# Performance work log

Hardware: AMD Instinct MI355X
Metric: run time of the kernel (lower is better)

Reference implementation:

```python
import jax, jax.numpy as jnp
import numpy as np

DIM = 256
DQK = DIM // 8
LN_SHAPE = (256, 4, 32, 32)


def setup_inputs() -> dict:
    key = jax.random.key(0)
    ks = jax.random.split(key, 12)
    B, C, Z, H, W = 4, 256, 4, 32, 32
    s = 0.02
    return {
        "x": jax.random.normal(ks[0], (B, C, Z, H, W), jnp.float32),
        "y": jax.random.normal(ks[1], (B, C, Z, H, W), jnp.float32),
        "Wq": jax.random.normal(ks[2], (DQK, C), jnp.float32) * s,
        "bq": jnp.zeros((DQK,), jnp.float32),
        "Wk": jax.random.normal(ks[3], (DQK, C), jnp.float32) * s,
        "bk": jnp.zeros((DQK,), jnp.float32),
        "Wv": jax.random.normal(ks[4], (C, C), jnp.float32) * s,
        "bv": jnp.zeros((C,), jnp.float32),
        "W1": jax.random.normal(ks[5], (C, C), jnp.float32) * s,
        "b1": jnp.zeros((C,), jnp.float32),
        "W2": jax.random.normal(ks[6], (C, C), jnp.float32) * s,
        "b2": jnp.zeros((C,), jnp.float32),
        "gamma": jnp.ones(LN_SHAPE, jnp.float32),
        "beta": jnp.zeros(LN_SHAPE, jnp.float32),
    }


def reference(x, y, Wq, bq, Wk, bk, Wv, bv, W1, b1, W2, b2, gamma, beta):
    B, C, Z, H, W = x.shape
    N = Z * H * W
    scale = (C // 8) ** (-0.5)

    def proj(t, Wm, bm):  # 1x1x1 conv3d == channel linear: [B,C,N] -> [B,out,N]
        return jnp.einsum('oc,bcn->bon', Wm, t.reshape(B, C, N)) + bm[None, :, None]

    def branch(a, b):
        q = proj(a, Wq, bq).transpose(0, 2, 1) * scale  # [B,N,dqk]
        k = proj(b, Wk, bk)                             # [B,dqk,N]
        v = proj(b, Wv, bv)                             # [B,C,N]
        attn = jax.nn.softmax(jnp.einsum('bnd,bdm->bnm', q, k), axis=-1)  # [B,N,N]
        out = jnp.einsum('bcm,bnm->bcn', v, attn).reshape(B, C, Z, H, W)
        h = out.transpose(0, 2, 3, 4, 1)  # [B,Z,H,W,C]
        h = jnp.maximum(jnp.einsum('bzhwc,oc->bzhwo', h, W1) + b1, 0.0)
        h = jnp.einsum('bzhwc,oc->bzhwo', h, W2) + b2
        h = h.transpose(0, 4, 1, 2, 3)  # [B,C,Z,H,W]
        mu = h.mean(axis=(1, 2, 3, 4), keepdims=True)
        var = h.var(axis=(1, 2, 3, 4), keepdims=True)
        return (h - mu) / jnp.sqrt(var + 1e-5) * gamma + beta

    return branch(x, y), branch(y, x)
```

## Files before the change

kernel.cpp:

```cpp
#include <hip/hip_runtime.h>

#define C_DIM 256
#define N_TOK 4096
#define DQK_  32
#define SCALE_Q 0.17677669529663687f

typedef unsigned short u16;
typedef __attribute__((ext_vector_type(8))) short bf16x8;
typedef __attribute__((ext_vector_type(16))) float f32x16;

__device__ __forceinline__ u16 f2b(float f) {
  unsigned u = __builtin_bit_cast(unsigned, f);
  unsigned r = (u + 0x7fffu + ((u >> 16) & 1u)) >> 16;
  return (u16)r;
}
__device__ __forceinline__ unsigned splitw(float v) {
  unsigned h = f2b(v);
  float hf = __builtin_bit_cast(float, h << 16);
  unsigned l = f2b(v - hf);
  return h | (l << 16);
}
__device__ __forceinline__ unsigned cvtpk(float lo, float hi) {
  unsigned r;
  asm("v_cvt_pk_bf16_f32 %0, %1, %2" : "=v"(r) : "v"(lo), "v"(hi));
// ... 113 lines not shown
      bf16x8 ah1 = *(const bf16x8*)(ldsAh + (lw + 32 + l31)*128 + (ko ^ swz));
      bf16x8 bh0 = *(const bf16x8*)(ldsBh + (sw + l31)*128      + (ko ^ swz));
      bf16x8 bh1 = *(const bf16x8*)(ldsBh + (sw + 32 + l31)*128 + (ko ^ swz));
      bf16x8 bl0 = *(const bf16x8*)(ldsBl + (sw + l31)*128      + (ko ^ swz));
      bf16x8 bl1 = *(const bf16x8*)(ldsBl + (sw + 32 + l31)*128 + (ko ^ swz));
      acc[0][0] = __builtin_amdgcn_mfma_f32_32x32x16_bf16(ah0, bh0, acc[0][0], 0,0,0);
      acc[0][1] = __builtin_amdgcn_mfma_f32_32x32x16_bf16(ah0, bh1, acc[0][1], 0,0,0);
      acc[1][0] = __builtin_amdgcn_mfma_f32_32x32x16_bf16(ah1, bh0, acc[1][0], 0,0,0);
      acc[1][1] = __builtin_amdgcn_mfma_f32_32x32x16_bf16(ah1, bh1, acc[1][1], 0,0,0);
      acc[0][0] = __builtin_amdgcn_mfma_f32_32x32x16_bf16(ah0, bl0, acc[0][0], 0,0,0);
      acc[0][1] = __builtin_amdgcn_mfma_f32_32x32x16_bf16(ah0, bl1, acc[0][1], 0,0,0);
      acc[1][0] = __builtin_amdgcn_mfma_f32_32x32x16_bf16(ah1, bl0, acc[1][0], 0,0,0);
      acc[1][1] = __builtin_amdgcn_mfma_f32_32x32x16_bf16(ah1, bl1, acc[1][1], 0,0,0);
    }
  }

  for (int h = 0; h < 2; ++h) {
    __syncthreads();
    if ((w >> 1) == h) {
      #pragma unroll
      for (int j = 0; j < 2; ++j) {
        int sl = j*32 + l31;
        float bv = bias[s0 + h*64 + sl];
        #pragma unroll
        for (int i = 0; i < 2; ++i)
          #pragma unroll
          for (int q = 0; q < 4; ++q) {
            int lbase = lw + i*32 + 8*q + 4*g;
            unsigned w0 = (unsigned)f2b(acc[i][j][q*4+0] + bv)
                        | ((unsigned)f2b(acc[i][j][q*4+1] + bv) << 16);
            unsigned w1 = (unsigned)f2b(acc[i][j][q*4+2] + bv)
                        | ((unsigned)f2b(acc[i][j][q*4+3] + bv) << 16);
            *(uint2*)(lds + sl*272 + lbase*2) = make_uint2(w0, w1);
          }
      }
    }
    __syncthreads();
    #pragma unroll
    for (int p = 0; p < 4; ++p) {
      int s = p*16 + (t >> 4), col = (t & 15)*8;
      uint4 v = *(const uint4*)(lds + s*272 + col*2);
      *(uint4*)(Ob + (size_t)(s0 + h*64 + s)*(size_t)N_TOK + l0 + col) = v;
    }
  }
}

__device__ __forceinline__ void proj_qk_body(
    char* lds, int bx, int which, int bb,
    const u16* __restrict__ xs_hi, const u16* __restrict__ ys_hi,
    const u16* __restrict__ Wqh, const u16* __restrict__ Wql,
    const u16* __restrict__ Wkh, const u16* __restrict__ Wkl,
    const float* __restrict__ bq, const float* __restrict__ bk,
    u16* __restrict__ Qout, u16* __restrict__ Kout)
{
  int branch = bb >> 2, batch = bb & 3;
  int n0 = bx * 256;
  const u16* Asrc = (which == 0 ? (branch ? ys_hi : xs_hi) : (branch ? xs_hi : ys_hi))
                    + (size_t)batch * N_TOK * C_DIM;
  const u16* Bh = which ? Wkh : Wqh;
  const u16* Bl = which ? Wkl : Wql;
  const float* bias = which ? bk : bq;
  float sc = which ? 1.0f : SCALE_Q;
  u16* out = (which ? Kout : Qout) + (size_t)bb * N_TOK * DQK_;

  char* ldsA  = lds;
  char* ldsBh = lds + 32768;
  char* ldsBl = lds + 40960;

  int t = threadIdx.x, w = t >> 6, lane = t & 63, g = lane >> 5, l31 = lane & 31;
  int swz = (l31 & 7) << 4;

  f32x16 acc[2];
  #pragma unroll
  for (int i = 0; i < 2; ++i)
    #pragma unroll
    for (int r = 0; r < 16; ++r) acc[i][r] = 0.f;

  uint4 rA[8]; uint4 rBh, rBl;
  #pragma unroll
  for (int c = 0; c < 8; ++c) {
    int idx = c*256 + t, row = idx >> 3, slot = idx & 7;
    rA[c] = *(const uint4*)(Asrc + (size_t)(n0 + row)*C_DIM + slot*8);
  }
  { int row = t >> 3, slot = t & 7;
    rBh = *(const uint4*)(Bh + (size_t)row*C_DIM + slot*8);
    rBl = *(const uint4*)(Bl + (size_t)row*C_DIM + slot*8); }

  for (int bk = 0; bk < 4; ++bk) {
    __syncthreads();
    #pragma unroll
    for (int c = 0; c < 8; ++c) {
      int idx = c*256 + t, row = idx >> 3, slot = idx & 7;
      *(uint4*)(ldsA + row*128 + ((slot*16) ^ ((row & 7) << 4))) = rA[c];
    }
    { int row = t >> 3, slot = t & 7;
      int off = row*128 + ((slot*16) ^ ((row & 7) << 4));
      *(uint4*)(ldsBh + off) = rBh;
      *(uint4*)(ldsBl + off) = rBl; }
    __syncthreads();
    if (bk < 3) {
      #pragma unroll
      for (int c = 0; c < 8; ++c) {
        int idx = c*256 + t, row = idx >> 3, slot = idx & 7;
        rA[c] = *(const uint4*)(Asrc + (size_t)(n0 + row)*C_DIM + (bk+1)*64 + slot*8);
      }
      { int row = t >> 3, slot = t & 7;
        rBh = *(const uint4*)(Bh + (size_t)row*C_DIM + (bk+1)*64 + slot*8);
        rBl = *(const uint4*)(Bl + (size_t)row*C_DIM + (bk+1)*64 + slot*8); }
    }
    #pragma unroll
    for (int ks = 0; ks < 4; ++ks) {
      int ko = ks*32 + g*16;
      bf16x8 a0 = *(const bf16x8*)(ldsA + (w*64 + l31)*128      + (ko ^ swz));
      bf16x8 a1 = *(const bf16x8*)(ldsA + (w*64 + 32 + l31)*128 + (ko ^ swz));
      bf16x8 bh = *(const bf16x8*)(ldsBh + l31*128 + (ko ^ swz));
      bf16x8 bl = *(const bf16x8*)(ldsBl + l31*128 + (ko ^ swz));
      acc[0] = __builtin_amdgcn_mfma_f32_32x32x16_bf16(a0, bh, acc[0], 0,0,0);
      acc[1] = __builtin_amdgcn_mfma_f32_32x32x16_bf16(a1, bh, acc[1], 0,0,0);
      acc[0] = __builtin_amdgcn_mfma_f32_32x32x16_bf16(a0, bl, acc[0], 0,0,0);
      acc[1] = __builtin_amdgcn_mfma_f32_32x32x16_bf16(a1, bl, acc[1], 0,0,0);
    }
  }
  float bv = bias[l31];
  #pragma unroll
  for (int sub = 0; sub < 2; ++sub)
    #pragma unroll
    for (int r = 0; r < 16; ++r) {
      int n = w*64 + sub*32 + (r&3) + 8*(r>>2) + 4*g;
      out[(size_t)(n0 + n)*DQK_ + l31] = f2b((acc[sub][r] + bv) * sc);
    }
}

__global__ __launch_bounds__(256) void pv_qk_kernel(
    const u16* __restrict__ xs_hi, const u16* __restrict__ ys_hi,
    const u16* __restrict__ Wvh, const u16* __restrict__ Wvl,
    const u16* __restrict__ Wqh, const u16* __restrict__ Wql,
    const u16* __restrict__ Wkh, const u16* __restrict__ Wkl,
    const float* __restrict__ bv, const float* __restrict__ bq, const float* __restrict__ bk,
    u16* __restrict__ Vt, u16* __restrict__ Qout, u16* __restrict__ Kout)
{
  __shared__ __align__(16) char lds[49152];
  int bid = blockIdx.x;
  const size_t AS = (size_t)N_TOK * C_DIM;
  if (bid < 512) {
    int bx = bid & 31, by = (bid >> 5) & 1, bb = bid >> 6;
    gemm_v_body(lds, bx, by, bb, ys_hi, xs_hi, AS, Wvh, Wvl, bv, Vt, AS);
  } else {
    int pb = bid - 512;
    int bx = pb & 15, which = (pb >> 4) & 1, bb = pb >> 5;
    proj_qk_body(lds, bx, which, bb, xs_hi, ys_hi, Wqh, Wql, Wkh, Wkl, bq, bk, Qout, Kout);
  }
}

__global__ __launch_bounds__(512) void attn_ffn_kernel(
    const u16* __restrict__ Qg, const u16* __restrict__ Kg,
    const u16* __restrict__ Vtg,
    const u16* __restrict__ W1h, const u16* __restrict__ W1l,
    const u16* __restrict__ W2h, const u16* __restrict__ W2l,
    const float* __restrict__ b1, const float* __restrict__ b2,
    float* __restrict__ out, float* __restrict__ part)
{
  __shared__ __align__(16) char lds[147456];
  int id = blockIdx.x;
  int bb = id & 7;
  int n0 = (id >> 3) * 128;
  const u16* Qb = Qg + (size_t)bb * N_TOK * DQK_;
  const u16* Kb = Kg + (size_t)bb * N_TOK * DQK_;
  const u16* Vb = Vtg + (size_t)bb * C_DIM * N_TOK;

  u16* Kl = (u16*)lds;
  u16* Vl = (u16*)(lds + 16384);

  int t = threadIdx.x;
  int w = t >> 6;
  int grp = w >> 2;
  int wg = w & 3;
  int t4 = t & 255;
  int lane = t & 63, g = lane >> 5, l31 = lane & 31;
  int swz = (l31 & 7) << 4;

  bf16x8 qf0 = *(const bf16x8*)(Qb + (size_t)(n0 + wg*32 + l31)*DQK_ + g*8);
  bf16x8 qf1 = *(const bf16x8*)(Qb + (size_t)(n0 + wg*32 + l31)*DQK_ + 16 + g*8);

  f32x16 acc[8];
  #pragma unroll
  for (int ct = 0; ct < 8; ++ct)
    #pragma unroll
    for (int r = 0; r < 16; ++r) acc[ct][r] = 0.f;

  float L = 0.f;

  bf16x8 stK, stV[8];
  const u16* kSrc = Kb + (size_t)(grp*32*64 + (t4>>7)*32 + (t4&31))*DQK_
                       + ((t4>>6)&1)*16 + ((t4>>5)&1)*8;
  const int vCol0 = grp*32*64;
  stK = *(const bf16x8*)(kSrc);
  #pragma unroll
  for (int i = 0; i < 8; ++i) {
    int q = i*256 + t4;
    stV[i] = *(const bf16x8*)(Vb + (size_t)(q >> 3)*N_TOK + vCol0 + (q & 7)*8);
  }

  u16* VlG = Vl + grp*32768;

  *(bf16x8*)(Kl + grp*4096 + t4*8) = stK;
  #pragma unroll
  for (int i = 0; i < 8; ++i) {
    int q = i*256 + t4;
    int c = q >> 3, slot = q & 7;
    *(bf16x8*)((char*)VlG + c*256 + ((slot*16) ^ ((c & 15) << 4))) = stV[i];
  }
  __syncthreads();

  int h = 0;
  for (int mt = 0; mt < 32; ++mt) {
    const u16* KlG = Kl + grp*4096 + h*2048;
    f32x16 z;
    #pragma unroll
    for (int r = 0; r < 16; ++r) z[r] = 0.f;
    bf16x8 ka = *(const bf16x8*)(KlG + (0*64 + lane)*8);
    bf16x8 kb = *(const bf16x8*)(KlG + (1*64 + lane)*8);
    bf16x8 kc = *(const bf16x8*)(KlG + (2*64 + lane)*8);
    bf16x8 kd = *(const bf16x8*)(KlG + (3*64 + lane)*8);
    f32x16 st0 = __builtin_amdgcn_mfma_f32_32x32x16_bf16(ka, qf0, z, 0,0,0);
    st0 = __builtin_amdgcn_mfma_f32_32x32x16_bf16(kb, qf1, st0, 0,0,0);
    f32x16 st1 = __builtin_amdgcn_mfma_f32_32x32x16_bf16(kc, qf0, z, 0,0,0);
    st1 = __builtin_amdgcn_mfma_f32_32x32x16_bf16(kd, qf1, st1, 0,0,0);

    if (mt + 1 < 32) {
      stK = *(const bf16x8*)(kSrc + (size_t)(mt+1)*64*DQK_);
      #pragma unroll
      for (int i = 0; i < 8; ++i) {
        int q = i*256 + t4;
        stV[i] = *(const bf16x8*)(Vb + (size_t)(q >> 3)*N_TOK + vCol0 + (mt+1)*64 + (q & 7)*8);
      }
    }

    float ps = 0.f;
    uint4 pav[4];
    #pragma unroll
    for (int msub = 0; msub < 2; ++msub) {
      f32x16 sv = msub ? st1 : st0;
      float p[16];
      #pragma unroll
      for (int r = 0; r < 16; ++r)
        p[r] = __expf(fminf(sv[r], 30.f));
      float q0 = (p[0]+p[1]) + (p[2]+p[3]);
      float q1 = (p[4]+p[5]) + (p[6]+p[7]);
      float q2 = (p[8]+p[9]) + (p[10]+p[11]);
      float q3 = (p[12]+p[13]) + (p[14]+p[15]);
      ps += (q0+q1) + (q2+q3);
      unsigned k0a = cvtpk(p[0],  p[1]),  k0b = cvtpk(p[2],  p[3]);
      unsigned k1a = cvtpk(p[4],  p[5]),  k1b = cvtpk(p[6],  p[7]);
      unsigned k2a = cvtpk(p[8],  p[9]),  k2b = cvtpk(p[10], p[11]);
      unsigned k3a = cvtpk(p[12], p[13]), k3b = cvtpk(p[14], p[15]);
      unsigned X1a = g ? k0a : k1a, X1b = g ? k0b : k1b;
      unsigned X2a = g ? k2a : k3a, X2b = g ? k2b : k3b;
      X1a = __shfl_xor(X1a, 32); X1b = __shfl_xor(X1b, 32);
      X2a = __shfl_xor(X2a, 32); X2b = __shfl_xor(X2b, 32);
      pav[msub*2]     = g ? make_uint4(X1a, X1b, k1a, k1b)
                          : make_uint4(k0a, k0b, X1a, X1b);
      pav[msub*2 + 1] = g ? make_uint4(X2a, X2b, k3a, k3b)
                          : make_uint4(k2a, k2b, X2a, X2b);
    }
    ps += __shfl_xor(ps, 32);
    L += ps;

    __builtin_amdgcn_s_setprio(1);
    #pragma unroll
    for (int ks = 0; ks < 4; ++ks) {
      bf16x8 pa = __builtin_bit_cast(bf16x8, pav[ks]);
      #pragma unroll
      for (int ct = 0; ct < 8; ++ct) {
        bf16x8 vv = *(const bf16x8*)((char*)VlG + (ct*32 + l31)*256
                     + ((h*128 + ks*32 + g*16) ^ ((l31 & 15) << 4)));
        acc[ct] = __builtin_amdgcn_mfma_f32_32x32x16_bf16(pa, vv, acc[ct], 0,0,0);
      }
    }
    __builtin_amdgcn_s_setprio(0);

    if (mt + 1 < 32) {
      *(bf16x8*)(Kl + grp*4096 + (h^1)*2048 + t4*8) = stK;
      #pragma unroll
      for (int i = 0; i < 8; ++i) {
        int q = i*256 + t4;
        int c = q >> 3, slot = q & 7;
        *(bf16x8*)((char*)VlG + c*256 + (((h ^ 1)*128 + slot*16) ^ ((c & 15) << 4))) = stV[i];
      }
    }
    __syncthreads();
    h ^= 1;
  }

  float* mb = (float*)Kl;
  mb[t] = L;
  __syncthreads();
  float Ln = L + mb[t ^ 256];

  float* vb = (float*)Vl;
  #pragma unroll
  for (int pass = 0; pass < 2; ++pass) {
    __syncthreads();
    if (grp == 1) {
      #pragma unroll
      for (int cc = 0; cc < 4; ++cc) {
        int ct = pass*4 + cc;
        #pragma unroll
        for (int r = 0; r < 16; ++r)
          vb[(cc*256 + t4)*16 + r] = acc[ct][r];
      }
    }
    __syncthreads();
    if (grp == 0) {
      #pragma unroll
      for (int cc = 0; cc < 4; ++cc) {
        int ct = pass*4 + cc;
        #pragma unroll
        for (int r = 0; r < 16; ++r)
          acc[ct][r] += vb[(cc*256 + t4)*16 + r];
      }
    }
  }
  __syncthreads();

  char* ldsO = lds + 16384;
  if (grp == 0) {
    float lr = 1.0f / Ln;
    float lrr[16];
    #pragma unroll
    for (int r = 0; r < 16; ++r)
      lrr[r] = __shfl(lr, (r&3) + 8*(r>>2) + 4*g, 32);
    #pragma unroll
    for (int ct = 0; ct < 8; ++ct) {
      #pragma unroll
      for (int r = 0; r < 16; ++r) {
        int n = wg*32 + (r&3) + 8*(r>>2) + 4*g;
        int c = ct*32 + l31;
        *(u16*)(ldsO + n*512 + ((c*2) ^ ((n & 7) << 4))) = f2b(acc[ct][r] * lrr[r]);
      }
    }
  }
  __syncthreads();

  int lw = (w & 1) * 64, sw = (w >> 1) * 64;
  char* ldsH1  = lds + 81920;
  char* ldsBh1 = lds + 81920;
  char* ldsBl1 = lds + 114688;
  char* ldsBh2 = lds + 16384;
  char* ldsBl2 = lds + 49152;

  f32x16 fa[2][2];
  #pragma unroll
  for (int i = 0; i < 2; ++i)
    #pragma unroll
    for (int j = 0; j < 2; ++j)
      #pragma unroll
      for (int r = 0; r < 16; ++r) fa[i][j][r] = 0.f;

  uint4 rBh[4], rBl[4];
  #pragma unroll
  for (int c = 0; c < 4; ++c) {
    int u = c*512 + t, row = u >> 3, slot = u & 7;
    rBh[c] = *(const uint4*)(W1h + (size_t)row*C_DIM + slot*8);
    rBl[c] = *(const uint4*)(W1l + (size_t)row*C_DIM + slot*8);
  }
  for (int bk = 0; bk < 4; ++bk) {
    __syncthreads();
    #pragma unroll
    for (int c = 0; c < 4; ++c) {
      int u = c*512 + t, row = u >> 3, slot = u & 7;
      int off = row*128 + ((slot*16) ^ ((row & 7) << 4));
      *(uint4*)(ldsBh1 + off) = rBh[c];
      *(uint4*)(ldsBl1 + off) = rBl[c];
    }
    __syncthreads();
    if (bk < 3) {
      #pragma unroll
      for (int c = 0; c < 4; ++c) {
        int u = c*512 + t, row = u >> 3, slot = u & 7;
        rBh[c] = *(const uint4*)(W1h + (size_t)row*C_DIM + (bk+1)*64 + slot*8);
        rBl[c] = *(const uint4*)(W1l + (size_t)row*C_DIM + (bk+1)*64 + slot*8);
      }
    }
    #pragma unroll
    for (int ks = 0; ks < 4; ++ks) {
      int ko = ks*32 + g*16;
      int kb = bk*128 + ko;
      bf16x8 ah0 = *(const bf16x8*)(ldsO + (lw + l31)*512      + (kb ^ swz));
      bf16x8 ah1 = *(const bf16x8*)(ldsO + (lw + 32 + l31)*512 + (kb ^ swz));
      bf16x8 bh0 = *(const bf16x8*)(ldsBh1 + (sw + l31)*128      + (ko ^ swz));
      bf16x8 bh1 = *(const bf16x8*)(ldsBh1 + (sw + 32 + l31)*128 + (ko ^ swz));
      bf16x8 bl0 = *(const bf16x8*)(ldsBl1 + (sw + l31)*128      + (ko ^ swz));
      bf16x8 bl1 = *(const bf16x8*)(ldsBl1 + (sw + 32 + l31)*128 + (ko ^ swz));
      fa[0][0] = __builtin_amdgcn_mfma_f32_32x32x16_bf16(ah0, bh0, fa[0][0], 0,0,0);
      fa[0][1] = __builtin_amdgcn_mfma_f32_32x32x16_bf16(ah0, bh1, fa[0][1], 0,0,0);
      fa[1][0] = __builtin_amdgcn_mfma_f32_32x32x16_bf16(ah1, bh0, fa[1][0], 0,0,0);
      fa[1][1] = __builtin_amdgcn_mfma_f32_32x32x16_bf16(ah1, bh1, fa[1][1], 0,0,0);
      fa[0][0] = __builtin_amdgcn_mfma_f32_32x32x16_bf16(ah0, bl0, fa[0][0], 0,0,0);
      fa[0][1] = __builtin_amdgcn_mfma_f32_32x32x16_bf16(ah0, bl1, fa[0][1], 0,0,0);
      fa[1][0] = __builtin_amdgcn_mfma_f32_32x32x16_bf16(ah1, bl0, fa[1][0], 0,0,0);
      fa[1][1] = __builtin_amdgcn_mfma_f32_32x32x16_bf16(ah1, bl1, fa[1][1], 0,0,0);
    }
  }
  __syncthreads();

  #pragma unroll
  for (int j = 0; j < 2; ++j) {
    int o = sw + j*32 + l31;
    float bvv = b1[o];
    #pragma unroll
    for (int i = 0; i < 2; ++i)
      #pragma unroll
      for (int r = 0; r < 16; ++r) {
        int n = lw + i*32 + (r&3) + 8*(r>>2) + 4*g;
        *(u16*)(ldsH1 + n*512 + ((o*2) ^ ((n & 7) << 4))) = f2b(fmaxf(fa[i][j][r] + bvv, 0.f));
      }
  }

  #pragma unroll
  for (int i = 0; i < 2; ++i)
    #pragma unroll
    for (int j = 0; j < 2; ++j)
      #pragma unroll
      for (int r = 0; r < 16; ++r) fa[i][j][r] = 0.f;

  #pragma unroll
  for (int c = 0; c < 4; ++c) {
    int u = c*512 + t, row = u >> 3, slot = u & 7;
    rBh[c] = *(const uint4*)(W2h + (size_t)row*C_DIM + slot*8);
    rBl[c] = *(const uint4*)(W2l + (size_t)row*C_DIM + slot*8);
  }
  for (int bk = 0; bk < 4; ++bk) {
    __syncthreads();
    #pragma unroll
    for (int c = 0; c < 4; ++c) {
      int u = c*512 + t, row = u >> 3, slot = u & 7;
      int off = row*128 + ((slot*16) ^ ((row & 7) << 4));
      *(uint4*)(ldsBh2 + off) = rBh[c];
      *(uint4*)(ldsBl2 + off) = rBl[c];
    }
    __syncthreads();
    if (bk < 3) {
      #pragma unroll
      for (int c = 0; c < 4; ++c) {
        int u = c*512 + t, row = u >> 3, slot = u & 7;
        rBh[c] = *(const uint4*)(W2h + (size_t)row*C_DIM + (bk+1)*64 + slot*8);
        rBl[c] = *(const uint4*)(W2l + (size_t)row*C_DIM + (bk+1)*64 + slot*8);
      }
    }
    #pragma unroll
    for (int ks = 0; ks < 4; ++ks) {
      int ko = ks*32 + g*16;
      int kb = bk*128 + ko;
      bf16x8 ah0 = *(const bf16x8*)(ldsH1 + (lw + l31)*512      + (kb ^ swz));
      bf16x8 ah1 = *(const bf16x8*)(ldsH1 + (lw + 32 + l31)*512 + (kb ^ swz));
      bf16x8 bh0 = *(const bf16x8*)(ldsBh2 + (sw + l31)*128      + (ko ^ swz));
      bf16x8 bh1 = *(const bf16x8*)(ldsBh2 + (sw + 32 + l31)*128 + (ko ^ swz));
      bf16x8 bl0 = *(const bf16x8*)(ldsBl2 + (sw + l31)*128      + (ko ^ swz));
      bf16x8 bl1 = *(const bf16x8*)(ldsBl2 + (sw + 32 + l31)*128 + (ko ^ swz));
      fa[0][0] = __builtin_amdgcn_mfma_f32_32x32x16_bf16(ah0, bh0, fa[0][0], 0,0,0);
      fa[0][1] = __builtin_amdgcn_mfma_f32_32x32x16_bf16(ah0, bh1, fa[0][1], 0,0,0);
      fa[1][0] = __builtin_amdgcn_mfma_f32_32x32x16_bf16(ah1, bh0, fa[1][0], 0,0,0);
      fa[1][1] = __builtin_amdgcn_mfma_f32_32x32x16_bf16(ah1, bh1, fa[1][1], 0,0,0);
      fa[0][0] = __builtin_amdgcn_mfma_f32_32x32x16_bf16(ah0, bl0, fa[0][0], 0,0,0);
      fa[0][1] = __builtin_amdgcn_mfma_f32_32x32x16_bf16(ah0, bl1, fa[0][1], 0,0,0);
      fa[1][0] = __builtin_amdgcn_mfma_f32_32x32x16_bf16(ah1, bl0, fa[1][0], 0,0,0);
      fa[1][1] = __builtin_amdgcn_mfma_f32_32x32x16_bf16(ah1, bl1, fa[1][1], 0,0,0);
    }
  }

  float s = 0.f, s2 = 0.f;
  #pragma unroll
  for (int j = 0; j < 2; ++j) {
    float bvv = b2[sw + j*32 + l31];
    #pragma unroll
    for (int i = 0; i < 2; ++i)
      #pragma unroll
      for (int r = 0; r < 16; ++r) {
        fa[i][j][r] += bvv;
        s += fa[i][j][r];
        s2 += fa[i][j][r]*fa[i][j][r];
      }
  }
  for (int off = 32; off; off >>= 1) {
    s  += __shfl_down(s, off, 64);
    s2 += __shfl_down(s2, off, 64);
  }
  __syncthreads();
  float* sc = (float*)lds;
  if (lane == 0) { sc[w*2] = s; sc[w*2+1] = s2; }
  __syncthreads();
  if (t == 0) {
    int slot = bb*32 + (id >> 3);
    float S = 0.f, S2 = 0.f;
    #pragma unroll
    for (int q = 0; q < 8; ++q) { S += sc[q*2]; S2 += sc[q*2+1]; }
    part[slot*2]     = S;
    part[slot*2 + 1] = S2;
  }

  float* Ob = out + (size_t)bb * (size_t)N_TOK * C_DIM;
  int l0 = n0;
  for (int qp = 0; qp < 4; ++qp) {
    __syncthreads();
    if ((w >> 1) == qp) {
      #pragma unroll
      for (int j = 0; j < 2; ++j) {
        int sl = j*32 + l31;
        #pragma unroll
        for (int i = 0; i < 2; ++i)
          #pragma unroll
          for (int q = 0; q < 4; ++q) {
            int lbase = lw + i*32 + 8*q + 4*g;
            float4 vv;
            vv.x = fa[i][j][q*4+0];
            vv.y = fa[i][j][q*4+1];
            vv.z = fa[i][j][q*4+2];
            vv.w = fa[i][j][q*4+3];
            *(float4*)(ldsO + sl*528 + lbase*4) = vv;
          }
      }
    }
    __syncthreads();
    #pragma unroll
    for (int p2 = 0; p2 < 4; ++p2) {
      int idx = p2*512 + t;
      int sl = idx >> 5, col = (idx & 31)*4;
      float4 v = *(const float4*)(ldsO + sl*528 + col*4);
      *(float4*)(Ob + (size_t)(qp*64 + sl)*(size_t)N_TOK + l0 + col) = v;
    }
  }
}

__global__ __launch_bounds__(256) void ln_apply_kernel(
    float* __restrict__ H, const float* __restrict__ gamma,
    const float* __restrict__ beta, const float* __restrict__ part)
{
  __shared__ float st[2];
  int base = blockIdx.x * 4096;
  int bb = base >> 20;
  int t = threadIdx.x;
  if (t < 64) {
    float s = 0.f, s2 = 0.f;
    if (t < 32) { s = part[(bb*32 + t)*2]; s2 = part[(bb*32 + t)*2 + 1]; }
    for (int off = 16; off; off >>= 1) {
      s  += __shfl_down(s, off, 64);
      s2 += __shfl_down(s2, off, 64);
    }
    if (t == 0) {
      float mean = s * (1.0f/1048576.0f);
      float var  = s2 * (1.0f/1048576.0f) - mean*mean;
      st[0] = mean;
      st[1] = rsqrtf(var + 1e-5f);
    }
  }
  __syncthreads();
  float mean = st[0], istd = st[1];
  #pragma unroll
  for (int k = 0; k < 4; ++k) {
    int e = base + (k*256 + t)*4;
    int rem = e & ((1 << 20) - 1);
    float4 h = *(float4*)(H + (size_t)e);
    float4 g = *(const float4*)(gamma + rem);
    float4 b = *(const float4*)(beta + rem);
    h.x = (h.x - mean)*istd*g.x + b.x;
    h.y = (h.y - mean)*istd*g.y + b.y;
    h.z = (h.z - mean)*istd*g.z + b.z;
    h.w = (h.w - mean)*istd*g.w + b.w;
    *(float4*)(H + (size_t)e) = h;
  }
}

extern "C" void kernel_launch(void* const* d_in, const int* in_sizes, int n_in,
                              void* d_out, int out_size, void* d_ws, size_t ws_size,
                              hipStream_t stream) {
  (void)in_sizes; (void)n_in; (void)out_size; (void)ws_size;
  const float* x  = (const float*)d_in[0];
  const float* y  = (const float*)d_in[1];
  const float* Wq = (const float*)d_in[2];
  const float* bq = (const float*)d_in[3];
  const float* Wk = (const float*)d_in[4];
  const float* bk = (const float*)d_in[5];
  const float* Wv = (const float*)d_in[6];
  const float* bv = (const float*)d_in[7];
  const float* W1 = (const float*)d_in[8];
  const float* b1 = (const float*)d_in[9];
  const float* W2 = (const float*)d_in[10];
  const float* b2 = (const float*)d_in[11];
  const float* gamma = (const float*)d_in[12];
  const float* beta  = (const float*)d_in[13];
  float* out = (float*)d_out;

  char* ws = (char*)d_ws;
  u16* xs_hi = (u16*)(ws);
  u16* ys_hi = (u16*)(ws + (8ull<<20));
  u16* Q     = (u16*)(ws + (16ull<<20));
  u16* Kp    = (u16*)(ws + (18ull<<20));
  u16* Vt    = (u16*)(ws + (20ull<<20));
  u16* Wvh   = (u16*)(ws + (52ull<<20));
  u16* Wvl   = Wvh + 65536;
  u16* W1h   = Wvh + 2*65536;
  u16* W1l   = Wvh + 3*65536;
  u16* W2h   = Wvh + 4*65536;
  u16* W2l   = Wvh + 5*65536;
  u16* Wqh   = Wvh + 6*65536;
  u16* Wql   = Wqh + 8192;
  u16* Wkh   = Wqh + 2*8192;
  u16* Wkl   = Wqh + 3*8192;
  float* part  = (float*)(ws + (53ull<<20));

  prep_kernel <<<2880, 256, 0, stream>>>(
      x, y, xs_hi, ys_hi, Wv, W1, W2, Wq, Wk,
      Wvh, Wvl, W1h, W1l, W2h, W2l, Wqh, Wql, Wkh, Wkl);
  pv_qk_kernel<<<768, 256, 0, stream>>>(
      xs_hi, ys_hi, Wvh, Wvl, Wqh, Wql, Wkh, Wkl, bv, bq, bk, Vt, Q, Kp);
  attn_ffn_kernel<<<256, 512, 0, stream>>>(
      Q, Kp, Vt, W1h, W1l, W2h, W2l, b1, b2, out, part);
  ln_apply_kernel <<<2048, 256, 0, stream>>>(out, gamma, beta, part);
}
```

Baseline: 218.3 us.

## Halve attention-FFN query tile to 64 tokens and double grid for occupancy

```diff
diff --git a/kernel.cpp b/kernel.cpp
--- a/kernel.cpp
+++ b/kernel.cpp
@@ -289,7 +289,7 @@
   }
 }
 
-__global__ __launch_bounds__(512) void attn_ffn_kernel(
+__global__ __launch_bounds__(512, 4) void attn_ffn_kernel(
     const u16* __restrict__ Qg, const u16* __restrict__ Kg,
     const u16* __restrict__ Vtg,
     const u16* __restrict__ W1h, const u16* __restrict__ W1l,
@@ -297,132 +297,134 @@
     const float* __restrict__ b1, const float* __restrict__ b2,
     float* __restrict__ out, float* __restrict__ part)
 {
-  __shared__ __align__(16) char lds[147456];
+  __shared__ __align__(16) char lds[73728];
   int id = blockIdx.x;
   int bb = id & 7;
-  int n0 = (id >> 3) * 128;
+  int tile = id >> 3;
+  int n0 = tile * 64;
   const u16* Qb = Qg + (size_t)bb * N_TOK * DQK_;
   const u16* Kb = Kg + (size_t)bb * N_TOK * DQK_;
   const u16* Vb = Vtg + (size_t)bb * C_DIM * N_TOK;
 
   u16* Kl = (u16*)lds;
-  u16* Vl = (u16*)(lds + 16384);
+  u16* Vl = (u16*)(lds + 8192);
 
   int t = threadIdx.x;
   int w = t >> 6;
   int grp = w >> 2;
-  int wg = w & 3;
+  int ch  = (w >> 1) & 1;
+  int qs  = w & 1;
   int t4 = t & 255;
   int lane = t & 63, g = lane >> 5, l31 = lane & 31;
-  int swz = (l31 & 7) << 4;
-
-  bf16x8 qf0 = *(const bf16x8*)(Qb + (size_t)(n0 + wg*32 + l31)*DQK_ + g*8);
-  bf16x8 qf1 = *(const bf16x8*)(Qb + (size_t)(n0 + wg*32 + l31)*DQK_ + 16 + g*8);
-
-  f32x16 acc[8];
-  #pragma unroll
-  for (int ct = 0; ct < 8; ++ct)
+
+  bf16x8 qf0 = *(const bf16x8*)(Qb + (size_t)(n0 + qs*32 + l31)*DQK_ + g*8);
+  bf16x8 qf1 = *(const bf16x8*)(Qb + (size_t)(n0 + qs*32 + l31)*DQK_ + 16 + g*8);
+
+  f32x16 acc[4];
+  #pragma unroll
+  for (int ct = 0; ct < 4; ++ct)
     #pragma unroll
     for (int r = 0; r < 16; ++r) acc[ct][r] = 0.f;
 
   float L = 0.f;
 
-  bf16x8 stK, stV[8];
-  const u16* kSrc = Kb + (size_t)(grp*32*64 + (t4>>7)*32 + (t4&31))*DQK_
-                       + ((t4>>6)&1)*16 + ((t4>>5)&1)*8;
-  const int vCol0 = grp*32*64;
-  stK = *(const bf16x8*)(kSrc);
-  #pragma unroll
-  for (int i = 0; i < 8; ++i) {
+  int kchunk = t4 >> 1, khalf = t4 & 1;
+  const u16* kSrc = Kb + (size_t)(grp*2048 + (kchunk & 31))*DQK_
+                      + ((kchunk>>6)&1)*16 + ((kchunk>>5)&1)*8 + khalf*4;
+  const int vCol0 = grp*2048;
+  u16* KlG0 = Kl + grp*2048;
+  u16* VlG  = Vl + grp*16384;
+
+  uint2 stK = *(const uint2*)(kSrc);
+  uint4 stV[4];
+  #pragma unroll
+  for (int i = 0; i < 4; ++i) {
     int q = i*256 + t4;
-    stV[i] = *(const bf16x8*)(Vb + (size_t)(q >> 3)*N_TOK + vCol0 + (q & 7)*8);
-  }
-
-  u16* VlG = Vl + grp*32768;
-
-  *(bf16x8*)(Kl + grp*4096 + t4*8) = stK;
-  #pragma unroll
-  for (int i = 0; i < 8; ++i) {
+    int c = q >> 2, slot = q & 3;
+    stV[i] = *(const uint4*)(Vb + (size_t)c*N_TOK + vCol0 + slot*8);
+  }
+
+  *(uint2*)(KlG0 + kchunk*8 + khalf*4) = stK;
+  #pragma unroll
+  for (int i = 0; i < 4; ++i) {
     int q = i*256 + t4;
-    int c = q >> 3, slot = q & 7;
-    *(bf16x8*)((char*)VlG + c*256 + ((slot*16) ^ ((c & 15) << 4))) = stV[i];
+    int c = q >> 2, slot = q & 3;
+    *(uint4*)((char*)VlG + c*128 + ((slot*16) ^ ((c & 7) << 4))) = stV[i];
   }
   __syncthreads();
 
   int h = 0;
-  for (int mt = 0; mt < 32; ++mt) {
-    const u16* KlG = Kl + grp*4096 + h*2048;
+  for (int mt = 0; mt < 64; ++mt) {
+    const u16* KlG = KlG0 + h*1024;
     f32x16 z;
     #pragma unroll
     for (int r = 0; r < 16; ++r) z[r] = 0.f;
-    bf16x8 ka = *(const bf16x8*)(KlG + (0*64 + lane)*8);
-    bf16x8 kb = *(const bf16x8*)(KlG + (1*64 + lane)*8);
-    bf16x8 kc = *(const bf16x8*)(KlG + (2*64 + lane)*8);
-    bf16x8 kd = *(const bf16x8*)(KlG + (3*64 + lane)*8);
+    bf16x8 ka = *(const bf16x8*)(KlG + lane*8);
+    bf16x8 kb = *(const bf16x8*)(KlG + (64 + lane)*8);
     f32x16 st0 = __builtin_amdgcn_mfma_f32_32x32x16_bf16(ka, qf0, z, 0,0,0);
     st0 = __builtin_amdgcn_mfma_f32_32x32x16_bf16(kb, qf1, st0, 0,0,0);
-    f32x16 st1 = __builtin_amdgcn_mfma_f32_32x32x16_bf16(kc, qf0, z, 0,0,0);
-    st1 = __builtin_amdgcn_mfma_f32_32x32x16_bf16(kd, qf1, st1, 0,0,0);
-
-    if (mt + 1 < 32) {
-      stK = *(const bf16x8*)(kSrc + (size_t)(mt+1)*64*DQK_);
-      #pragma unroll
-      for (int i = 0; i < 8; ++i) {
+
+    if (mt + 1 < 64) {
+      stK = *(const uint2*)(kSrc + (size_t)(mt+1)*32*DQK_);
+      #pragma unroll
+      for (int i = 0; i < 4; ++i) {
         int q = i*256 + t4;
-        stV[i] = *(const bf16x8*)(Vb + (size_t)(q >> 3)*N_TOK + vCol0 + (mt+1)*64 + (q & 7)*8);
-      }
-    }
-
-    float ps = 0.f;
-    uint4 pav[4];
-    #pragma unroll
-    for (int msub = 0; msub < 2; ++msub) {
-      f32x16 sv = msub ? st1 : st0;
-      float p[16];
-      #pragma unroll
-      for (int r = 0; r < 16; ++r)
-        p[r] = __expf(fminf(sv[r], 30.f));
-      float q0 = (p[0]+p[1]) + (p[2]+p[3]);
-      float q1 = (p[4]+p[5]) + (p[6]+p[7]);
-      float q2 = (p[8]+p[9]) + (p[10]+p[11]);
-      float q3 = (p[12]+p[13]) + (p[14]+p[15]);
-      ps += (q0+q1) + (q2+q3);
-      unsigned k0a = cvtpk(p[0],  p[1]),  k0b = cvtpk(p[2],  p[3]);
-      unsigned k1a = cvtpk(p[4],  p[5]),  k1b = cvtpk(p[6],  p[7]);
-      unsigned k2a = cvtpk(p[8],  p[9]),  k2b = cvtpk(p[10], p[11]);
-      unsigned k3a = cvtpk(p[12], p[13]), k3b = cvtpk(p[14], p[15]);
+        int c = q >> 2, slot = q & 3;
+        stV[i] = *(const uint4*)(Vb + (size_t)c*N_TOK + vCol0 + (mt+1)*32 + slot*8);
+      }
+    }
+
+    float ps;
+    uint4 pav[2];
+    {
+      float p0 = __expf(fminf(st0[0], 30.f)),  p1 = __expf(fminf(st0[1], 30.f));
+      float p2 = __expf(fminf(st0[2], 30.f)),  p3 = __expf(fminf(st0[3], 30.f));
+      unsigned k0a = cvtpk(p0, p1), k0b = cvtpk(p2, p3);
+      float s01 = (p0+p1) + (p2+p3);
+      float p4 = __expf(fminf(st0[4], 30.f)),  p5 = __expf(fminf(st0[5], 30.f));
+      float p6 = __expf(fminf(st0[6], 30.f)),  p7 = __expf(fminf(st0[7], 30.f));
+      unsigned k1a = cvtpk(p4, p5), k1b = cvtpk(p6, p7);
+      float s23 = (p4+p5) + (p6+p7);
+      float p8 = __expf(fminf(st0[8], 30.f)),  p9 = __expf(fminf(st0[9], 30.f));
+      float pa2 = __expf(fminf(st0[10], 30.f)), pb2 = __expf(fminf(st0[11], 30.f));
+      unsigned k2a = cvtpk(p8, p9), k2b = cvtpk(pa2, pb2);
+      float s45 = (p8+p9) + (pa2+pb2);
+      float pc2 = __expf(fminf(st0[12], 30.f)), pd2 = __expf(fminf(st0[13], 30.f));
+      float pe2 = __expf(fminf(st0[14], 30.f)), pf2 = __expf(fminf(st0[15], 30.f));
+      unsigned k3a = cvtpk(pc2, pd2), k3b = cvtpk(pe2, pf2);
+      float s67 = (pc2+pd2) + (pe2+pf2);
+      ps = (s01 + s23) + (s45 + s67);
       unsigned X1a = g ? k0a : k1a, X1b = g ? k0b : k1b;
       unsigned X2a = g ? k2a : k3a, X2b = g ? k2b : k3b;
       X1a = __shfl_xor(X1a, 32); X1b = __shfl_xor(X1b, 32);
       X2a = __shfl_xor(X2a, 32); X2b = __shfl_xor(X2b, 32);
-      pav[msub*2]     = g ? make_uint4(X1a, X1b, k1a, k1b)
-                          : make_uint4(k0a, k0b, X1a, X1b);
-      pav[msub*2 + 1] = g ? make_uint4(X2a, X2b, k3a, k3b)
-                          : make_uint4(k2a, k2b, X2a, X2b);
+      pav[0] = g ? make_uint4(X1a, X1b, k1a, k1b) : make_uint4(k0a, k0b, X1a, X1b);
+      pav[1] = g ? make_uint4(X2a, X2b, k3a, k3b) : make_uint4(k2a, k2b, X2a, X2b);
     }
     ps += __shfl_xor(ps, 32);
     L += ps;
 
     __builtin_amdgcn_s_setprio(1);
     #pragma unroll
-    for (int ks = 0; ks < 4; ++ks) {
+    for (int ks = 0; ks < 2; ++ks) {
       bf16x8 pa = __builtin_bit_cast(bf16x8, pav[ks]);
       #pragma unroll
-      for (int ct = 0; ct < 8; ++ct) {
-        bf16x8 vv = *(const bf16x8*)((char*)VlG + (ct*32 + l31)*256
-                     + ((h*128 + ks*32 + g*16) ^ ((l31 & 15) << 4)));
+      for (int ct = 0; ct < 4; ++ct) {
+        int cr = ch*128 + ct*32 + l31;
+        bf16x8 vv = *(const bf16x8*)((char*)VlG + cr*128
+                     + ((h*64 + ks*32 + g*16) ^ ((l31 & 7) << 4)));
         acc[ct] = __builtin_amdgcn_mfma_f32_32x32x16_bf16(pa, vv, acc[ct], 0,0,0);
       }
     }
     __builtin_amdgcn_s_setprio(0);
 
-    if (mt + 1 < 32) {
-      *(bf16x8*)(Kl + grp*4096 + (h^1)*2048 + t4*8) = stK;
-      #pragma unroll
-      for (int i = 0; i < 8; ++i) {
+    if (mt + 1 < 64) {
+      *(uint2*)(KlG0 + (h^1)*1024 + kchunk*8 + khalf*4) = stK;
+      #pragma unroll
+      for (int i = 0; i < 4; ++i) {
         int q = i*256 + t4;
-        int c = q >> 3, slot = q & 7;
-        *(bf16x8*)((char*)VlG + c*256 + (((h ^ 1)*128 + slot*16) ^ ((c & 15) << 4))) = stV[i];
+        int c = q >> 2, slot = q & 3;
+        *(uint4*)((char*)VlG + c*128 + (((h^1)*64 + slot*16) ^ ((c & 7) << 4))) = stV[i];
       }
     }
     __syncthreads();
@@ -430,37 +432,28 @@
   }
 
   float* mb = (float*)Kl;
+  float* vb = (float*)Vl;
   mb[t] = L;
+  if (grp == 1) {
+    #pragma unroll
+    for (int ct = 0; ct < 4; ++ct)
+      #pragma unroll
+      for (int r = 0; r < 16; ++r)
+        vb[(ct*256 + t4)*16 + r] = acc[ct][r];
+  }
   __syncthreads();
-  float Ln = L + mb[t ^ 256];
-
-  float* vb = (float*)Vl;
-  #pragma unroll
-  for (int pass = 0; pass < 2; ++pass) {
-    __syncthreads();
-    if (grp == 1) {
-      #pragma unroll
-      for (int cc = 0; cc < 4; ++cc) {
-        int ct = pass*4 + cc;
-        #pragma unroll
-        for (int r = 0; r < 16; ++r)
-          vb[(cc*256 + t4)*16 + r] = acc[ct][r];
-      }
-    }
-    __syncthreads();
-    if (grp == 0) {
-      #pragma unroll
-      for (int cc = 0; cc < 4; ++cc) {
-        int ct = pass*4 + cc;
-        #pragma unroll
-        for (int r = 0; r < 16; ++r)
-          acc[ct][r] += vb[(cc*256 + t4)*16 + r];
-      }
-    }
+  float Ln = 1.f;
+  if (grp == 0) {
+    Ln = L + mb[t ^ 256];
+    #pragma unroll
+    for (int ct = 0; ct < 4; ++ct)
+      #pragma unroll
+      for (int r = 0; r < 16; ++r)
+        acc[ct][r] += vb[(ct*256 + t4)*16 + r];
   }
   __syncthreads();
 
-  char* ldsO = lds + 16384;
+  char* ldsO = lds + 8192;
   if (grp == 0) {
     float lr = 1.0f / Ln;
     float lrr[16];
@@ -468,156 +461,135 @@
     for (int r = 0; r < 16; ++r)
       lrr[r] = __shfl(lr, (r&3) + 8*(r>>2) + 4*g, 32);
     #pragma unroll
-    for (int ct = 0; ct < 8; ++ct) {
+    for (int ct = 0; ct < 4; ++ct) {
       #pragma unroll
       for (int r = 0; r < 16; ++r) {
-        int n = wg*32 + (r&3) + 8*(r>>2) + 4*g;
-        int c = ct*32 + l31;
+        int n = qs*32 + (r&3) + 8*(r>>2) + 4*g;
+        int c = ch*128 + ct*32 + l31;
         *(u16*)(ldsO + n*512 + ((c*2) ^ ((n & 7) << 4))) = f2b(acc[ct][r] * lrr[r]);
       }
     }
   }
   __syncthreads();
 
-  int lw = (w & 1) * 64, sw = (w >> 1) * 64;
-  char* ldsH1  = lds + 81920;
-  char* ldsBh1 = lds + 81920;
-  char* ldsBl1 = lds + 114688;
-  char* ldsBh2 = lds + 16384;
-  char* ldsBl2 = lds + 49152;
-
-  f32x16 fa[2][2];
-  #pragma unroll
-  for (int i = 0; i < 2; ++i)
-    #pragma unroll
-    for (int j = 0; j < 2; ++j)
-      #pragma unroll
-      for (int r = 0; r < 16; ++r) fa[i][j][r] = 0.f;
-
-  uint4 rBh[4], rBl[4];
-  #pragma unroll
-  for (int c = 0; c < 4; ++c) {
-    int u = c*512 + t, row = u >> 3, slot = u & 7;
-    rBh[c] = *(const uint4*)(W1h + (size_t)row*C_DIM + slot*8);
-    rBl[c] = *(const uint4*)(W1l + (size_t)row*C_DIM + slot*8);
-  }
-  for (int bk = 0; bk < 4; ++bk) {
-    __syncthreads();
-    #pragma unroll
-    for (int c = 0; c < 4; ++c) {
-      int u = c*512 + t, row = u >> 3, slot = u & 7;
-      int off = row*128 + ((slot*16) ^ ((row & 7) << 4));
-      *(uint4*)(ldsBh1 + off) = rBh[c];
-      *(uint4*)(ldsBl1 + off) = rBl[c];
-    }
-    __syncthreads();
-    if (bk < 3) {
-      #pragma unroll
-      for (int c = 0; c < 4; ++c) {
-        int u = c*512 + t, row = u >> 3, slot = u & 7;
-        rBh[c] = *(const uint4*)(W1h + (size_t)row*C_DIM + (bk+1)*64 + slot*8);
-        rBl[c] = *(const uint4*)(W1l + (size_t)row*C_DIM + (bk+1)*64 + slot*8);
-      }
-    }
-    #pragma unroll
-    for (int ks = 0; ks < 4; ++ks) {
+  int lw = w & 1, sq = w >> 1;
+  char* ldsWh = lds + 40960;
+  char* ldsWl = lds + 57344;
+  char* ldsH1 = lds + 8192;
+  int swz3 = (l31 & 3) << 4;
+  int swz7 = (l31 & 7) << 4;
+
+  f32x16 fa[2];
+  #pragma unroll
+  for (int j = 0; j < 2; ++j)
+    #pragma unroll
+    for (int r = 0; r < 16; ++r) fa[j][r] = 0.f;
+
+  uint4 rWh[2], rWl[2];
+  #pragma unroll
+  for (int c2 = 0; c2 < 2; ++c2) {
+    int u = c2*512 + t, s = u >> 2, slot = u & 3;
+    rWh[c2] = *(const uint4*)(W1h + (size_t)s*C_DIM + slot*8);
+    rWl[c2] = *(const uint4*)(W1l + (size_t)s*C_DIM + slot*8);
+  }
+  for (int bk = 0; bk < 8; ++bk) {
+    __syncthreads();
+    #pragma unroll
+    for (int c2 = 0; c2 < 2; ++c2) {
+      int u = c2*512 + t, s = u >> 2, slot = u & 3;
+      int off = s*64 + ((slot*16) ^ ((s & 3) << 4));
+      *(uint4*)(ldsWh + off) = rWh[c2];
+      *(uint4*)(ldsWl + off) = rWl[c2];
+    }
+    __syncthreads();
+    if (bk < 7) {
+      #pragma unroll
+      for (int c2 = 0; c2 < 2; ++c2) {
+        int u = c2*512 + t, s = u >> 2, slot = u & 3;
+        rWh[c2] = *(const uint4*)(W1h + (size_t)s*C_DIM + (bk+1)*32 + slot*8);
+        rWl[c2] = *(const uint4*)(W1l + (size_t)s*C_DIM + (bk+1)*32 + slot*8);
+      }
+    }
+    #pragma unroll
+    for (int ks = 0; ks < 2; ++ks) {
       int ko = ks*32 + g*16;
-      int kb = bk*128 + ko;
-      bf16x8 ah0 = *(const bf16x8*)(ldsO + (lw + l31)*512      + (kb ^ swz));
-      bf16x8 ah1 = *(const bf16x8*)(ldsO + (lw + 32 + l31)*512 + (kb ^ swz));
-      bf16x8 bh0 = *(const bf16x8*)(ldsBh1 + (sw + l31)*128      + (ko ^ swz));
-      bf16x8 bh1 = *(const bf16x8*)(ldsBh1 + (sw + 32 + l31)*128 + (ko ^ swz));
-      bf16x8 bl0 = *(const bf16x8*)(ldsBl1 + (sw + l31)*128      + (ko ^ swz));
-      bf16x8 bl1 = *(const bf16x8*)(ldsBl1 + (sw + 32 + l31)*128 + (ko ^ swz));
-      fa[0][0] = __builtin_amdgcn_mfma_f32_32x32x16_bf16(ah0, bh0, fa[0][0], 0,0,0);
-      fa[0][1] = __builtin_amdgcn_mfma_f32_32x32x16_bf16(ah0, bh1, fa[0][1], 0,0,0);
-      fa[1][0] = __builtin_amdgcn_mfma_f32_32x32x16_bf16(ah1, bh0, fa[1][0], 0,0,0);
-      fa[1][1] = __builtin_amdgcn_mfma_f32_32x32x16_bf16(ah1, bh1, fa[1][1], 0,0,0);
-      fa[0][0] = __builtin_amdgcn_mfma_f32_32x32x16_bf16(ah0, bl0, fa[0][0], 0,0,0);
-      fa[0][1] = __builtin_amdgcn_mfma_f32_32x32x16_bf16(ah0, bl1, fa[0][1], 0,0,0);
-      fa[1][0] = __builtin_amdgcn_mfma_f32_32x32x16_bf16(ah1, bl0, fa[1][0], 0,0,0);
-      fa[1][1] = __builtin_amdgcn_mfma_f32_32x32x16_bf16(ah1, bl1, fa[1][1], 0,0,0);
+      bf16x8 a0  = *(const bf16x8*)(ldsO + (lw*32 + l31)*512 + ((bk*64 + ko) ^ swz7));
+      bf16x8 bh0 = *(const bf16x8*)(ldsWh + (sq*64 + l31)*64      + (ko ^ swz3));
+      bf16x8 bh1 = *(const bf16x8*)(ldsWh + (sq*64 + 32 + l31)*64 + (ko ^ swz3));
+      bf16x8 bl0 = *(const bf16x8*)(ldsWl + (sq*64 + l31)*64      + (ko ^ swz3));
+      bf16x8 bl1 = *(const bf16x8*)(ldsWl + (sq*64 + 32 + l31)*64 + (ko ^ swz3));
+      fa[0] = __builtin_amdgcn_mfma_f32_32x32x16_bf16(a0, bh0, fa[0], 0,0,0);
+      fa[1] = __builtin_amdgcn_mfma_f32_32x32x16_bf16(a0, bh1, fa[1], 0,0,0);
+      fa[0] = __builtin_amdgcn_mfma_f32_32x32x16_bf16(a0, bl0, fa[0], 0,0,0);
+      fa[1] = __builtin_amdgcn_mfma_f32_32x32x16_bf16(a0, bl1, fa[1], 0,0,0);
     }
   }
   __syncthreads();
 
   #pragma unroll
-  for (int j = 0; j < 2; ++j) {
-    int o = sw + j*32 + l31;
-    float bvv = b1[o];
-    #pragma unroll
-    for (int i = 0; i < 2; ++i)
-      #pragma unroll
-      for (int r = 0; r < 16; ++r) {
-        int n = lw + i*32 + (r&3) + 8*(r>>2) + 4*g;
-        *(u16*)(ldsH1 + n*512 + ((o*2) ^ ((n & 7) << 4))) = f2b(fmaxf(fa[i][j][r] + bvv, 0.f));
-      }
-  }
-
-  #pragma unroll
-  for (int i = 0; i < 2; ++i)
-    #pragma unroll
-    for (int j = 0; j < 2; ++j)
-      #pragma unroll
-      for (int r = 0; r < 16; ++r) fa[i][j][r] = 0.f;
-
-  #pragma unroll
-  for (int c = 0; c < 4; ++c) {
-    int u = c*512 + t, row = u >> 3, slot = u & 7;
-    rBh[c] = *(const uint4*)(W2h + (size_t)row*C_DIM + slot*8);
-    rBl[c] = *(const uint4*)(W2l + (size_t)row*C_DIM + slot*8);
-  }
-  for (int bk = 0; bk < 4; ++bk) {
-    __syncthreads();
-    #pragma unroll
-    for (int c = 0; c < 4; ++c) {
-      int u = c*512 + t, row = u >> 3, slot = u & 7;
-      int off = row*128 + ((slot*16) ^ ((row & 7) << 4));
-      *(uint4*)(ldsBh2 + off) = rBh[c];
-      *(uint4*)(ldsBl2 + off) = rBl[c];
-    }
-    __syncthreads();
-    if (bk < 3) {
-      #pragma unroll
-      for (int c = 0; c < 4; ++c) {
-        int u = c*512 + t, row = u >> 3, slot = u & 7;
-        rBh[c] = *(const uint4*)(W2h + (size_t)row*C_DIM + (bk+1)*64 + slot*8);
-        rBl[c] = *(const uint4*)(W2l + (size_t)row*C_DIM + (bk+1)*64 + slot*8);
-      }
-    }
-    #pragma unroll
-    for (int ks = 0; ks < 4; ++ks) {
+  for (int jb = 0; jb < 2; ++jb) {
+    int s = sq*64 + jb*32 + l31;
+    float bvv = b1[s];
+    #pragma unroll
+    for (int r = 0; r < 16; ++r) {
+      int n = lw*32 + (r&3) + 8*(r>>2) + 4*g;
+      *(u16*)(ldsH1 + n*512 + ((s*2) ^ ((n & 7) << 4))) = f2b(fmaxf(fa[jb][r] + bvv, 0.f));
+    }
+  }
+  #pragma unroll
+  for (int j = 0; j < 2; ++j)
+    #pragma unroll
+    for (int r = 0; r < 16; ++r) fa[j][r] = 0.f;
+
+  #pragma unroll
+  for (int c2 = 0; c2 < 2; ++c2) {
+    int u = c2*512 + t, s = u >> 2, slot = u & 3;
+    rWh[c2] = *(const uint4*)(W2h + (size_t)s*C_DIM + slot*8);
+    rWl[c2] = *(const uint4*)(W2l + (size_t)s*C_DIM + slot*8);
+  }
+  for (int bk = 0; bk < 8; ++bk) {
+    __syncthreads();
+    #pragma unroll
+    for (int c2 = 0; c2 < 2; ++c2) {
+      int u = c2*512 + t, s = u >> 2, slot = u & 3;
+      int off = s*64 + ((slot*16) ^ ((s & 3) << 4));
+      *(uint4*)(ldsWh + off) = rWh[c2];
+      *(uint4*)(ldsWl + off) = rWl[c2];
+    }
+    __syncthreads();
+    if (bk < 7) {
+      #pragma unroll
+      for (int c2 = 0; c2 < 2; ++c2) {
+        int u = c2*512 + t, s = u >> 2, slot = u & 3;
+        rWh[c2] = *(const uint4*)(W2h + (size_t)s*C_DIM + (bk+1)*32 + slot*8);
+        rWl[c2] = *(const uint4*)(W2l + (size_t)s*C_DIM + (bk+1)*32 + slot*8);
+      }
+    }
+    #pragma unroll
+    for (int ks = 0; ks < 2; ++ks) {
       int ko = ks*32 + g*16;
-      int kb = bk*128 + ko;
-      bf16x8 ah0 = *(const bf16x8*)(ldsH1 + (lw + l31)*512      + (kb ^ swz));
-      bf16x8 ah1 = *(const bf16x8*)(ldsH1 + (lw + 32 + l31)*512 + (kb ^ swz));
-      bf16x8 bh0 = *(const bf16x8*)(ldsBh2 + (sw + l31)*128      + (ko ^ swz));
-      bf16x8 bh1 = *(const bf16x8*)(ldsBh2 + (sw + 32 + l31)*128 + (ko ^ swz));
-      bf16x8 bl0 = *(const bf16x8*)(ldsBl2 + (sw + l31)*128      + (ko ^ swz));
-      bf16x8 bl1 = *(const bf16x8*)(ldsBl2 + (sw + 32 + l31)*128 + (ko ^ swz));
-      fa[0][0] = __builtin_amdgcn_mfma_f32_32x32x16_bf16(ah0, bh0, fa[0][0], 0,0,0);
-      fa[0][1] = __builtin_amdgcn_mfma_f32_32x32x16_bf16(ah0, bh1, fa[0][1], 0,0,0);
-      fa[1][0] = __builtin_amdgcn_mfma_f32_32x32x16_bf16(ah1, bh0, fa[1][0], 0,0,0);
-      fa[1][1] = __builtin_amdgcn_mfma_f32_32x32x16_bf16(ah1, bh1, fa[1][1], 0,0,0);
-      fa[0][0] = __builtin_amdgcn_mfma_f32_32x32x16_bf16(ah0, bl0, fa[0][0], 0,0,0);
-      fa[0][1] = __builtin_amdgcn_mfma_f32_32x32x16_bf16(ah0, bl1, fa[0][1], 0,0,0);
-      fa[1][0] = __builtin_amdgcn_mfma_f32_32x32x16_bf16(ah1, bl0, fa[1][0], 0,0,0);
-      fa[1][1] = __builtin_amdgcn_mfma_f32_32x32x16_bf16(ah1, bl1, fa[1][1], 0,0,0);
+      bf16x8 a0  = *(const bf16x8*)(ldsH1 + (lw*32 + l31)*512 + ((bk*64 + ko) ^ swz7));
+      bf16x8 bh0 = *(const bf16x8*)(ldsWh + (sq*64 + l31)*64      + (ko ^ swz3));
+      bf16x8 bh1 = *(const bf16x8*)(ldsWh + (sq*64 + 32 + l31)*64 + (ko ^ swz3));
+      bf16x8 bl0 = *(const bf16x8*)(ldsWl + (sq*64 + l31)*64      + (ko ^ swz3));
+      bf16x8 bl1 = *(const bf16x8*)(ldsWl + (sq*64 + 32 + l31)*64 + (ko ^ swz3));
+      fa[0] = __builtin_amdgcn_mfma_f32_32x32x16_bf16(a0, bh0, fa[0], 0,0,0);
+      fa[1] = __builtin_amdgcn_mfma_f32_32x32x16_bf16(a0, bh1, fa[1], 0,0,0);
+      fa[0] = __builtin_amdgcn_mfma_f32_32x32x16_bf16(a0, bl0, fa[0], 0,0,0);
+      fa[1] = __builtin_amdgcn_mfma_f32_32x32x16_bf16(a0, bl1, fa[1], 0,0,0);
     }
   }
 
   float s = 0.f, s2 = 0.f;
   #pragma unroll
-  for (int j = 0; j < 2; ++j) {
-    float bvv = b2[sw + j*32 + l31];
-    #pragma unroll
-    for (int i = 0; i < 2; ++i)
-      #pragma unroll
-      for (int r = 0; r < 16; ++r) {
-        fa[i][j][r] += bvv;
-        s += fa[i][j][r];
-        s2 += fa[i][j][r]*fa[i][j][r];
-      }
+  for (int jb = 0; jb < 2; ++jb) {
+    float bvv = b2[sq*64 + jb*32 + l31];
+    #pragma unroll
+    for (int r = 0; r < 16; ++r) {
+      fa[jb][r] += bvv;
+      s += fa[jb][r];
+      s2 += fa[jb][r]*fa[jb][r];
+    }
   }
   for (int off = 32; off; off >>= 1) {
     s  += __shfl_down(s, off, 64);
@@ -628,7 +600,7 @@
   if (lane == 0) { sc[w*2] = s; sc[w*2+1] = s2; }
   __syncthreads();
   if (t == 0) {
-    int slot = bb*32 + (id >> 3);
+    int slot = bb*64 + tile;
     float S = 0.f, S2 = 0.f;
     #pragma unroll
     for (int q = 0; q < 8; ++q) { S += sc[q*2]; S2 += sc[q*2+1]; }
@@ -637,34 +609,32 @@
   }
 
   float* Ob = out + (size_t)bb * (size_t)N_TOK * C_DIM;
-  int l0 = n0;
+  char* ts = lds + 40960;
   for (int qp = 0; qp < 4; ++qp) {
     __syncthreads();
-    if ((w >> 1) == qp) {
-      #pragma unroll
-      for (int j = 0; j < 2; ++j) {
-        int sl = j*32 + l31;
+    if (sq == qp) {
+      #pragma unroll
+      for (int jb = 0; jb < 2; ++jb) {
+        int sl = jb*32 + l31;
         #pragma unroll
-        for (int i = 0; i < 2; ++i)
-          #pragma unroll
-          for (int q = 0; q < 4; ++q) {
-            int lbase = lw + i*32 + 8*q + 4*g;
-            float4 vv;
-            vv.x = fa[i][j][q*4+0];
-            vv.y = fa[i][j][q*4+1];
-            vv.z = fa[i][j][q*4+2];
-            vv.w = fa[i][j][q*4+3];
-            *(float4*)(ldsO + sl*528 + lbase*4) = vv;
-          }
-      }
-    }
-    __syncthreads();
-    #pragma unroll
-    for (int p2 = 0; p2 < 4; ++p2) {
+        for (int q2 = 0; q2 < 4; ++q2) {
+          int nbase = lw*32 + 8*q2 + 4*g;
+          float4 vv;
+          vv.x = fa[jb][q2*4+0];
+          vv.y = fa[jb][q2*4+1];
+          vv.z = fa[jb][q2*4+2];
+          vv.w = fa[jb][q2*4+3];
+          *(float4*)(ts + sl*272 + nbase*4) = vv;
+        }
+      }
+    }
+    __syncthreads();
+    #pragma unroll
+    for (int p2 = 0; p2 < 2; ++p2) {
       int idx = p2*512 + t;
-      int sl = idx >> 5, col = (idx & 31)*4;
-      float4 v = *(const float4*)(ldsO + sl*528 + col*4);
-      *(float4*)(Ob + (size_t)(qp*64 + sl)*(size_t)N_TOK + l0 + col) = v;
+      int sl = idx >> 4, col = (idx & 15)*4;
+      float4 v = *(const float4*)(ts + sl*272 + col*4);
+      *(float4*)(Ob + (size_t)(qp*64 + sl)*(size_t)N_TOK + n0 + col) = v;
     }
   }
 }
@@ -678,9 +648,9 @@
   int bb = base >> 20;
   int t = threadIdx.x;
   if (t < 64) {
-    float s = 0.f, s2 = 0.f;
-    if (t < 32) { s = part[(bb*32 + t)*2]; s2 = part[(bb*32 + t)*2 + 1]; }
-    for (int off = 16; off; off >>= 1) {
+    float s  = part[(bb*64 + t)*2];
+    float s2 = part[(bb*64 + t)*2 + 1];
+    for (int off = 32; off; off >>= 1) {
       s  += __shfl_down(s, off, 64);
       s2 += __shfl_down(s2, off, 64);
     }
@@ -751,7 +721,7 @@
       Wvh, Wvl, W1h, W1l, W2h, W2l, Wqh, Wql, Wkh, Wkl);
   pv_qk_kernel<<<768, 256, 0, stream>>>(
       xs_hi, ys_hi, Wvh, Wvl, Wqh, Wql, Wkh, Wkl, bv, bq, bk, Vt, Q, Kp);
-  attn_ffn_kernel<<<256, 512, 0, stream>>>(
+  attn_ffn_kernel<<<512, 512, 0, stream>>>(
       Q, Kp, Vt, W1h, W1l, W2h, W2l, b1, b2, out, part);
   ln_apply_kernel <<<2048, 256, 0, stream>>>(out, gamma, beta, part);
 }
```

Result: slower. 287.1 us (+31.5%).
